# Kernel optimization log

Hardware: AMD Instinct MI355X
Metric: run time of the kernel (lower is better)

The kernel has to match this reference:

```python
import jax, jax.numpy as jnp
import numpy as np

EMBED = 1024
HEADS = 16
HEAD_DIM = EMBED // HEADS


def setup_inputs() -> dict:
    key = jax.random.key(0)
    ks = jax.random.split(key, 9)
    s = 0.02
    x = jax.random.normal(ks[0], (2, 2048, EMBED), dtype=jnp.float32)
    Wq = jax.random.normal(ks[1], (EMBED, EMBED), dtype=jnp.float32) * s
    bq = jnp.zeros((EMBED,), dtype=jnp.float32)
    Wk = jax.random.normal(ks[2], (EMBED, EMBED), dtype=jnp.float32) * s
    bk = jnp.zeros((EMBED,), dtype=jnp.float32)
    Wv = jax.random.normal(ks[3], (EMBED, EMBED), dtype=jnp.float32) * s
    bv = jnp.zeros((EMBED,), dtype=jnp.float32)
    Wo = jax.random.normal(ks[4], (EMBED, EMBED), dtype=jnp.float32) * s
    bo = jnp.zeros((EMBED,), dtype=jnp.float32)
    return {"x": x, "Wq": Wq, "bq": bq, "Wk": Wk, "bk": bk,
            "Wv": Wv, "bv": bv, "Wo": Wo, "bo": bo}


def reference(x, Wq, bq, Wk, bk, Wv, bv, Wo, bo):
    B, S, E = x.shape
    H, D = HEADS, HEAD_DIM
    scale = jnp.sqrt(jnp.asarray(D, dtype=x.dtype))
    # projections (torch Linear: y = x @ W.T + b)
    q = (x @ Wq.T + bq).reshape(B, S, H, D).transpose(0, 2, 1, 3)  # [B,H,S,D]
    k = (x @ Wk.T + bk).reshape(B, S, H, D).transpose(0, 2, 1, 3)
    v = (x @ Wv.T + bv).reshape(B, S, H, D).transpose(0, 2, 1, 3)
    scores = jnp.einsum('bhqd,bhkd->bhqk', q, k) / scale  # [B,H,S,S]
    probs = jax.nn.softmax(scores, axis=-1)
    out = jnp.einsum('bhqk,bhkd->bhqd', probs, v)  # [B,H,S,D]
    out = out.transpose(0, 2, 1, 3).reshape(B, S, E)
    return out @ Wo.T + bo
```

## Files before the change

kernel.cpp:

```cpp
#include <hip/hip_runtime.h>
#include <cstddef>

#define EMBED 1024
#define HEADS 16
#define HDIM  64
#define BATCH 2
#define SEQ   2048
#define MTOT  (BATCH*SEQ)

typedef __attribute__((ext_vector_type(8)))  short short8;
typedef __attribute__((ext_vector_type(4)))  float f32x4;
typedef __attribute__((ext_vector_type(16))) float f32x16;

typedef __attribute__((address_space(1))) const unsigned int* gas_u32p;
typedef __attribute__((address_space(3))) unsigned int* las_u32p;

static __device__ __forceinline__ void gload_lds16(const void* g, void* l) {
    __builtin_amdgcn_global_load_lds((gas_u32p)g, (las_u32p)l, 16, 0, 0);
}

static __device__ __forceinline__ unsigned short f2bf(float x) {
    unsigned u = __builtin_bit_cast(unsigned, x);
    unsigned r = (u + 0x7FFFu + ((u >> 16) & 1u)) >> 16;
    return (unsigned short)r;
}

static __device__ __forceinline__ unsigned pk_bf16(float lo, float hi) {
    unsigned r;
    asm("v_cvt_pk_bf16_f32 %0, %1, %2" : "=v"(r) : "v"(lo), "v"(hi));
    return r;
}

static __device__ __forceinline__ void plane32_swap(unsigned &a, unsigned &b) {
    auto r = __builtin_amdgcn_permlane32_swap((int)a, (int)b, false, false);
    a = (unsigned)r[0];
    b = (unsigned)r[1];
}

static __device__ __forceinline__ f32x16 mfma32(short8 a, short8 b, f32x16 c) {
    return __builtin_amdgcn_mfma_f32_32x32x16_bf16(a, b, c, 0, 0, 0);
}

__global__ __launch_bounds__(256)
void convx(const float* __restrict__ x, unsigned short* __restrict__ xh)
{
    const size_t i = ((size_t)blockIdx.x * 256 + threadIdx.x) * 8;
    float4 a = *(const float4*)(x + i);
    float4 b = *(const float4*)(x + i + 4);
    unsigned short o[8] __attribute__((aligned(16)));
    o[0] = f2bf(a.x); o[1] = f2bf(a.y); o[2] = f2bf(a.z); o[3] = f2bf(a.w);
    o[4] = f2bf(b.x); o[5] = f2bf(b.y); o[6] = f2bf(b.z); o[7] = f2bf(b.w);
    *(uint4*)(xh + i) = *(const uint4*)o;
}

__global__ __launch_bounds__(256)
void convw(const float* __restrict__ Wq, const float* __restrict__ Wk,
           const float* __restrict__ Wv, const float* __restrict__ Wo,
           unsigned short* __restrict__ Wh)
{
    const int sel = blockIdx.y;
    const float* src = sel == 0 ? Wq : sel == 1 ? Wk : sel == 2 ? Wv : Wo;
    unsigned short* dst = Wh + (size_t)sel * EMBED * EMBED;
    const size_t i = ((size_t)blockIdx.x * 256 + threadIdx.x) * 4;
    float4 a = *(const float4*)(src + i);
    ushort4 o;
    o.x = f2bf(a.x); o.y = f2bf(a.y); o.z = f2bf(a.z); o.w = f2bf(a.w);
    *(ushort4*)(dst + i) = o;
}

__global__ __launch_bounds__(256)
void gemm_qkv_bf16(const unsigned short* __restrict__ A,
                   const unsigned short* __restrict__ Wqh,
                   const unsigned short* __restrict__ Wkh,
                   const unsigned short* __restrict__ Wvh,
                   const float* __restrict__ bq,
                   const float* __restrict__ bk,
                   const float* __restrict__ bv,
                   unsigned short* __restrict__ Qb,
                   unsigned short* __restrict__ Kb,
                   unsigned short* __restrict__ Vt)
{
    __shared__ short As[128 * 32];
    __shared__ short Bs[128 * 32];

    const int tid  = threadIdx.x;
    const int lane = tid & 63;
    const int w    = tid >> 6;
    const int c    = lane & 15;
    const int g    = lane >> 4;
    const int wr   = w >> 1;
    const int wc   = w & 1;

    const int m0   = blockIdx.y * 128;
    const int bx   = blockIdx.x;
    const int wsel = bx >> 3;
    const int n0   = (bx & 7) * 128;

    const unsigned short* W = (wsel == 0) ? Wqh : (wsel == 1) ? Wkh : Wvh;
    const float* bias       = (wsel == 0) ? bq  : (wsel == 1) ? bk  : bv;

    f32x4 acc[4][4] = {};

    for (int k0 = 0; k0 < EMBED; k0 += 32) {
        __syncthreads();
        #pragma unroll
        for (int i = 0; i < 2; ++i) {
            int s   = (w * 2 + i) * 64 + lane;
            int row = s >> 2;
            int k8  = (s & 3) * 8;
            gload_lds16(A + (size_t)(m0 + row) * EMBED + k0 + k8,
                        As + (size_t)(w * 2 + i) * 512);
            gload_lds16(W + (size_t)(n0 + row) * EMBED + k0 + k8,
                        Bs + (size_t)(w * 2 + i) * 512);
        }
        __syncthreads();

        short8 af[4], bf[4];
        #pragma unroll
        for (int mi = 0; mi < 4; ++mi)
            af[mi] = *(const short8*)&As[(wr * 64 + mi * 16 + c) * 32 + g * 8];
        #pragma unroll
        for (int ni = 0; ni < 4; ++ni)
            bf[ni] = *(const short8*)&Bs[(wc * 64 + ni * 16 + c) * 32 + g * 8];
        #pragma unroll
        for (int mi = 0; mi < 4; ++mi)
            #pragma unroll
            for (int ni = 0; ni < 4; ++ni)
                acc[mi][ni] = __builtin_amdgcn_mfma_f32_16x16x32_bf16(
                    af[mi], bf[ni], acc[mi][ni], 0, 0, 0);
    }

    if (wsel == 2) {
        #pragma unroll
        for (int mi = 0; mi < 4; ++mi) {
            const int m  = m0 + wr * 64 + mi * 16 + g * 4;
            const int bb = m >> 11;
            const int ss = m & (SEQ - 1);
            #pragma unroll
            for (int ni = 0; ni < 4; ++ni) {
                const int col = n0 + wc * 64 + ni * 16 + c;
                const int hh = col >> 6, dd = col & 63;
                const float bi_ = bias[col];
                ushort4 o;
                o.x = f2bf(acc[mi][ni][0] + bi_);
                o.y = f2bf(acc[mi][ni][1] + bi_);
                o.z = f2bf(acc[mi][ni][2] + bi_);
                o.w = f2bf(acc[mi][ni][3] + bi_);
                *(ushort4*)&Vt[((size_t)((bb * HEADS + hh) * HDIM) + dd) * SEQ + ss] = o;
            }
        }
    } else {
        unsigned short* Out = (wsel == 0) ? Qb : Kb;
        const float oscale  = (wsel == 0) ? 0.125f : 1.0f;
        #pragma unroll
        for (int mi = 0; mi < 4; ++mi)
            #pragma unroll
            for (int r = 0; r < 4; ++r) {
                const int m = m0 + wr * 64 + mi * 16 + g * 4 + r;
                #pragma unroll
                for (int ni = 0; ni < 4; ++ni) {
                    const int col = n0 + wc * 64 + ni * 16 + c;
                    Out[(size_t)m * EMBED + col] =
                        f2bf((acc[mi][ni][r] + bias[col]) * oscale);
                }
            }
    }
}

__global__ __launch_bounds__(256)
void gemm_o_bf16(const unsigned short* __restrict__ A,
                 const unsigned short* __restrict__ Woh,
                 const float* __restrict__ bo,
                 float* __restrict__ C)
{
    __shared__ short As[128 * 32];
    __shared__ short Bs[64 * 32];

    const int tid  = threadIdx.x;
    const int lane = tid & 63;
    const int w    = tid >> 6;
    const int c    = lane & 15;
    const int g    = lane >> 4;
    const int wr   = w >> 1;
    const int wc   = w & 1;

    const int m0 = blockIdx.y * 128;
    const int n0 = blockIdx.x * 64;

    f32x4 acc[4][2] = {};

    for (int k0 = 0; k0 < EMBED; k0 += 32) {
        __syncthreads();
        #pragma unroll
        for (int i = 0; i < 2; ++i) {
            int s   = (w * 2 + i) * 64 + lane;
            int row = s >> 2;
            int k8  = (s & 3) * 8;
            gload_lds16(A + (size_t)(m0 + row) * EMBED + k0 + k8,
                        As + (size_t)(w * 2 + i) * 512);
        }
        {
            int s   = w * 64 + lane;
            int row = s >> 2;
            int k8  = (s & 3) * 8;
            gload_lds16(Woh + (size_t)(n0 + row) * EMBED + k0 + k8,
                        Bs + (size_t)w * 512);
        }
        __syncthreads();

        short8 af[4], bf[2];
        #pragma unroll
        for (int mi = 0; mi < 4; ++mi)
            af[mi] = *(const short8*)&As[(wr * 64 + mi * 16 + c) * 32 + g * 8];
        #pragma unroll
        for (int ni = 0; ni < 2; ++ni)
            bf[ni] = *(const short8*)&Bs[(wc * 32 + ni * 16 + c) * 32 + g * 8];
        #pragma unroll
        for (int mi = 0; mi < 4; ++mi)
            #pragma unroll
            for (int ni = 0; ni < 2; ++ni)
                acc[mi][ni] = __builtin_amdgcn_mfma_f32_16x16x32_bf16(
                    af[mi], bf[ni], acc[mi][ni], 0, 0, 0);
    }

    #pragma unroll
    for (int mi = 0; mi < 4; ++mi)
        #pragma unroll
        for (int r = 0; r < 4; ++r) {
            const int m = m0 + wr * 64 + mi * 16 + g * 4 + r;
            #pragma unroll
            for (int ni = 0; ni < 2; ++ni) {
                const int col = n0 + wc * 32 + ni * 16 + c;
                C[(size_t)m * EMBED + col] = acc[mi][ni][r] + bo[col];
            }
        }
}

__global__ __launch_bounds__(512, 4)
void flash_attn_mfma3(const unsigned short* __restrict__ Qb,
                      const unsigned short* __restrict__ Kb,
                      const unsigned short* __restrict__ Vt,
                      unsigned short* __restrict__ O)
{
    __shared__ short KT[2][2][64 * 64];
    __shared__ short VT[2][2][64 * 64];

    const int tid  = threadIdx.x;
    const int lane = tid & 63;
    const int w    = tid >> 6;
    const int qt   = w & 3;
    const int half = w >> 2;
    const int l31  = lane & 31;
    const int hi   = lane >> 5;
    const int q0   = blockIdx.x * 128 + qt * 32;
    const int h    = blockIdx.y;
    const int b    = blockIdx.z;

    short8 qf[4];
    {
        const unsigned short* qrow =
            Qb + (size_t)(b * SEQ + q0 + l31) * EMBED + h * HDIM + hi * 8;
        #pragma unroll
        for (int kc = 0; kc < 4; ++kc)
            qf[kc] = *(const short8*)(qrow + kc * 16);
    }

    const int tb     = w >> 1;
    const int sthalf = tb >> 1;
    const int stV    = tb & 1;
    const int ssub   = w & 1;
    const int strow  = ssub * 32 + (lane >> 3);
    const int ch     = (lane & 7) ^ (strow & 7);
    const unsigned short* kS =
        Kb + (size_t)(b * SEQ + sthalf * (SEQ / 2) + strow) * EMBED + h * HDIM + ch * 8;
    const unsigned short* vS =
        Vt + ((size_t)((b * HEADS + h) * HDIM) + strow) * SEQ + sthalf * (SEQ / 2) + ch * 8;

    f32x16 acc[2] = {};
    float m_run = -1e30f, l_run = 0.f;

    #define STAGE(kt2, bb)                                                    \
        do {                                                                  \
            if (stV == 0) {                                                   \
                const unsigned short* src = kS + (size_t)(kt2) * 64 * EMBED;  \
                short* kd = &KT[sthalf][bb][ssub * 2048];                     \
                _Pragma("unroll")                                             \
                for (int it = 0; it < 4; ++it)                                \
                    gload_lds16(src + (size_t)it * 8 * EMBED, kd + it * 512); \
            } else {                                                          \
                const unsigned short* src = vS + (kt2) * 64;                  \
                short* vd = &VT[sthalf][bb][ssub * 2048];                     \
                _Pragma("unroll")                                             \
                for (int it = 0; it < 4; ++it)                                \
                    gload_lds16(src + (size_t)it * 8 * SEQ, vd + it * 512);   \
            }                                                                 \
        } while (0)

    STAGE(0, 0);
    __syncthreads();

    for (int kt = 0; kt < SEQ / 2 / 64; ++kt) {
        const int bi = kt & 1;
        if (kt < SEQ / 2 / 64 - 1) STAGE(kt + 1, bi ^ 1);

        const short* kb_ = &KT[half][bi][0];
        const short* vb_ = &VT[half][bi][0];

        f32x16 s[2] = {};
        #pragma unroll
        for (int t = 0; t < 2; ++t) {
            const int row = t * 32 + l31;
            const int rm  = l31 & 7;
            #pragma unroll
            for (int kc = 0; kc < 4; ++kc) {
                short8 ka = *(const short8*)&kb_[row * 64 + (((2 * kc + hi) ^ rm) * 8)];
                s[t] = mfma32(ka, qf[kc], s[t]);
            }
        }

        float mt = -1e30f;
        #pragma unroll
        for (int t = 0; t < 2; ++t)
            #pragma unroll
            for (int r = 0; r < 16; ++r)
                mt = fmaxf(mt, s[t][r]);
        mt = fmaxf(mt, __shfl_xor(mt, 32, 64));

        if (__any(mt > m_run + 8.f)) {
            float mnew  = fmaxf(m_run, mt);
            float alpha = __expf(m_run - mnew);
            m_run = mnew;
            l_run *= alpha;
            #pragma unroll
            for (int r = 0; r < 16; ++r) {
                const int qr = (r & 3) + 8 * (r >> 2) + 4 * hi;
                float af = __shfl(alpha, qr, 64);
                acc[0][r] *= af;
                acc[1][r] *= af;
            }
        }

        float rs = 0.f;
        #pragma unroll
        for (int t = 0; t < 2; ++t)
            #pragma unroll
            for (int r = 0; r < 16; ++r) {
                float pv = __expf(s[t][r] - m_run);
                s[t][r] = pv;
                rs += pv;
            }
        rs += __shfl_xor(rs, 32, 64);
        l_run += rs;

        short8 pf[2][2];
        #pragma unroll
        for (int t = 0; t < 2; ++t)
            #pragma unroll
            for (int kc = 0; kc < 2; ++kc) {
                unsigned A0 = pk_bf16(s[t][8 * kc + 0], s[t][8 * kc + 1]);
                unsigned A1 = pk_bf16(s[t][8 * kc + 2], s[t][8 * kc + 3]);
                unsigned B0 = pk_bf16(s[t][8 * kc + 4], s[t][8 * kc + 5]);
                unsigned B1 = pk_bf16(s[t][8 * kc + 6], s[t][8 * kc + 7]);
                plane32_swap(A0, B0);
                plane32_swap(A1, B1);
                uint4 fw = make_uint4(A0, A1, B0, B1);
                pf[t][kc] = __builtin_bit_cast(short8, fw);
            }

        #pragma unroll
        for (int dt = 0; dt < 2; ++dt) {
            const int row = dt * 32 + l31;
            const int rm  = l31 & 7;
            #pragma unroll
            for (int t = 0; t < 2; ++t)
                #pragma unroll
                for (int kc = 0; kc < 2; ++kc) {
                    short8 vf = *(const short8*)
                        &vb_[row * 64 + (((4 * t + 2 * kc + hi) ^ rm) * 8)];
                    acc[dt] = mfma32(pf[t][kc], vf, acc[dt]);
                }
        }

        __syncthreads();
    }
    #undef STAGE

    float* mrgf = (float*)&KT[0][0][0];
    float* mlbf = (float*)&VT[0][0][0];
    if (half == 1) {
        #pragma unroll
        for (int dt = 0; dt < 2; ++dt)
            #pragma unroll
            for (int r = 0; r < 16; ++r) {
                const int qr = (r & 3) + 8 * (r >> 2) + 4 * hi;
                mrgf[qt * 2048 + qr * 64 + dt * 32 + l31] = acc[dt][r];
            }
        if (lane < 32) {
            *(float2*)&mlbf[qt * 64 + lane * 2] = make_float2(m_run, l_run);
        }
    }
    __syncthreads();
    if (half == 0) {
        float2 ml = *(const float2*)&mlbf[qt * 64 + l31 * 2];
        float mx  = fmaxf(m_run, ml.x);
        float al  = __expf(m_run - mx);
        float ah  = __expf(ml.x - mx);
        float inv = 1.f / (l_run * al + ml.y * ah);
        float fl = al * inv, fh = ah * inv;
        #pragma unroll
        for (int r = 0; r < 16; ++r) {
            const int qr = (r & 3) + 8 * (r >> 2) + 4 * hi;
            float flr = __shfl(fl, qr, 64);
            float fhr = __shfl(fh, qr, 64);
            #pragma unroll
            for (int dt = 0; dt < 2; ++dt) {
                float oh  = mrgf[qt * 2048 + qr * 64 + dt * 32 + l31];
                float val = acc[dt][r] * flr + oh * fhr;
                O[(size_t)(b * SEQ + q0 + qr) * EMBED + h * HDIM + dt * 32 + l31]
                    = f2bf(val);
            }
        }
    }
}

extern "C" void kernel_launch(void* const* d_in, const int* in_sizes, int n_in,
                              void* d_out, int out_size, void* d_ws, size_t ws_size,
                              hipStream_t stream)
{
    const float* x  = (const float*)d_in[0];
    const float* Wq = (const float*)d_in[1];
    const float* bq = (const float*)d_in[2];
    const float* Wk = (const float*)d_in[3];
    const float* bk = (const float*)d_in[4];
    const float* Wv = (const float*)d_in[5];
    const float* bv = (const float*)d_in[6];
    const float* Wo = (const float*)d_in[7];
    const float* bo = (const float*)d_in[8];
    float* out = (float*)d_out;

    const size_t ME = (size_t)MTOT * EMBED;
    unsigned short* xh   = (unsigned short*)d_ws;
    unsigned short* Qb   = xh   + ME;
    unsigned short* Kb   = Qb   + ME;
    unsigned short* Vt   = Kb   + ME;
    unsigned short* attn = Vt   + ME;
    unsigned short* Wh   = attn + ME;

    dim3 blk(256);

    convx<<<dim3(MTOT * EMBED / 2048), blk, 0, stream>>>(x, xh);
    convw<<<dim3(EMBED * EMBED / 1024, 4), blk, 0, stream>>>(Wq, Wk, Wv, Wo, Wh);

    gemm_qkv_bf16<<<dim3(24, MTOT / 128), blk, 0, stream>>>(
        xh, Wh, Wh + (size_t)EMBED * EMBED, Wh + 2 * (size_t)EMBED * EMBED,
        bq, bk, bv, Qb, Kb, Vt);

    flash_attn_mfma3<<<dim3(SEQ / 128, HEADS, BATCH), dim3(512), 0, stream>>>(
        Qb, Kb, Vt, attn);

    gemm_o_bf16<<<dim3(EMBED / 64, MTOT / 128), blk, 0, stream>>>(
        attn, Wh + 3 * (size_t)EMBED * EMBED, bo, out);
}
```

Measured before the change: 133.8 us.

## Split attention KV range four ways per block and widen output GEMM tile

The attention kernel moves from 512 to 1024 threads per block. Each query tile is now split across four KV quarters of 512 keys, processed in 32-key steps. The partial softmax results are combined by a two-level tree merge through LDS, and s_setprio is raised around the MFMA sections. The output projection GEMM tile grows from 128x64 to 128x128, which halves its grid and raises reuse per block. The cost is more merge synchronization and register pressure, and occupancy changes with the larger block and the launch_bounds(1024,8) hint.

```diff
diff --git a/kernel.cpp b/kernel.cpp
--- a/kernel.cpp
+++ b/kernel.cpp
@@ -174,7 +174,7 @@
                  float* __restrict__ C)
 {
     __shared__ short As[128 * 32];
-    __shared__ short Bs[64 * 32];
+    __shared__ short Bs[128 * 32];
 
     const int tid  = threadIdx.x;
     const int lane = tid & 63;
@@ -185,9 +185,9 @@
     const int wc   = w & 1;
 
     const int m0 = blockIdx.y * 128;
-    const int n0 = blockIdx.x * 64;
-
-    f32x4 acc[4][2] = {};
+    const int n0 = blockIdx.x * 128;
+
+    f32x4 acc[4][4] = {};
 
     for (int k0 = 0; k0 < EMBED; k0 += 32) {
         __syncthreads();
@@ -198,27 +198,22 @@
             int k8  = (s & 3) * 8;
             gload_lds16(A + (size_t)(m0 + row) * EMBED + k0 + k8,
                         As + (size_t)(w * 2 + i) * 512);
-        }
-        {
-            int s   = w * 64 + lane;
-            int row = s >> 2;
-            int k8  = (s & 3) * 8;
             gload_lds16(Woh + (size_t)(n0 + row) * EMBED + k0 + k8,
-                        Bs + (size_t)w * 512);
+                        Bs + (size_t)(w * 2 + i) * 512);
         }
         __syncthreads();
 
-        short8 af[4], bf[2];
+        short8 af[4], bf[4];
         #pragma unroll
         for (int mi = 0; mi < 4; ++mi)
             af[mi] = *(const short8*)&As[(wr * 64 + mi * 16 + c) * 32 + g * 8];
         #pragma unroll
-        for (int ni = 0; ni < 2; ++ni)
-            bf[ni] = *(const short8*)&Bs[(wc * 32 + ni * 16 + c) * 32 + g * 8];
+        for (int ni = 0; ni < 4; ++ni)
+            bf[ni] = *(const short8*)&Bs[(wc * 64 + ni * 16 + c) * 32 + g * 8];
         #pragma unroll
         for (int mi = 0; mi < 4; ++mi)
             #pragma unroll
-            for (int ni = 0; ni < 2; ++ni)
+            for (int ni = 0; ni < 4; ++ni)
                 acc[mi][ni] = __builtin_amdgcn_mfma_f32_16x16x32_bf16(
                     af[mi], bf[ni], acc[mi][ni], 0, 0, 0);
     }
@@ -229,29 +224,31 @@
         for (int r = 0; r < 4; ++r) {
             const int m = m0 + wr * 64 + mi * 16 + g * 4 + r;
             #pragma unroll
-            for (int ni = 0; ni < 2; ++ni) {
-                const int col = n0 + wc * 32 + ni * 16 + c;
+            for (int ni = 0; ni < 4; ++ni) {
+                const int col = n0 + wc * 64 + ni * 16 + c;
                 C[(size_t)m * EMBED + col] = acc[mi][ni][r] + bo[col];
             }
         }
 }
 
-__global__ __launch_bounds__(512, 4)
-void flash_attn_mfma3(const unsigned short* __restrict__ Qb,
+__global__ __launch_bounds__(1024, 8)
+void flash_attn_mfma4(const unsigned short* __restrict__ Qb,
                       const unsigned short* __restrict__ Kb,
                       const unsigned short* __restrict__ Vt,
                       unsigned short* __restrict__ O)
 {
-    __shared__ short KT[2][2][64 * 64];
-    __shared__ short VT[2][2][64 * 64];
+    __shared__ short KT[4][2][32 * 64];
+    __shared__ short VS[4][2][32 * 64];
+    __shared__ float MLB[2][4][32][2];
 
     const int tid  = threadIdx.x;
     const int lane = tid & 63;
     const int w    = tid >> 6;
     const int qt   = w & 3;
-    const int half = w >> 2;
+    const int qr4  = w >> 2;
     const int l31  = lane & 31;
     const int hi   = lane >> 5;
+    const int rm   = l31 & 7;
     const int q0   = blockIdx.x * 128 + qt * 32;
     const int h    = blockIdx.y;
     const int b    = blockIdx.z;
@@ -265,65 +262,61 @@
             qf[kc] = *(const short8*)(qrow + kc * 16);
     }
 
-    const int tb     = w >> 1;
-    const int sthalf = tb >> 1;
-    const int stV    = tb & 1;
-    const int ssub   = w & 1;
-    const int strow  = ssub * 32 + (lane >> 3);
-    const int ch     = (lane & 7) ^ (strow & 7);
-    const unsigned short* kS =
-        Kb + (size_t)(b * SEQ + sthalf * (SEQ / 2) + strow) * EMBED + h * HDIM + ch * 8;
-    const unsigned short* vS =
-        Vt + ((size_t)((b * HEADS + h) * HDIM) + strow) * SEQ + sthalf * (SEQ / 2) + ch * 8;
+    const int stV  = (w >> 1) & 1;
+    const int ssub = w & 1;
+    const int r0   = ssub * 16 + (lane >> 3);
+    const int r1   = r0 + 8;
+    const int sl   = lane & 7;
+    const int c0   = sl ^ (r0 & 7);
+    const int c1   = sl ^ (r1 & 7);
+    const unsigned short* g0;
+    const unsigned short* g1;
+    if (stV == 0) {
+        g0 = Kb + (size_t)(b * SEQ + qr4 * 512 + r0) * EMBED + h * HDIM + c0 * 8;
+        g1 = Kb + (size_t)(b * SEQ + qr4 * 512 + r1) * EMBED + h * HDIM + c1 * 8;
+    } else {
+        const int d0 = r0 + 32 * (c0 >> 2), k0o = (c0 & 3) * 8;
+        const int d1 = r1 + 32 * (c1 >> 2), k1o = (c1 & 3) * 8;
+        g0 = Vt + ((size_t)((b * HEADS + h) * HDIM) + d0) * SEQ + qr4 * 512 + k0o;
+        g1 = Vt + ((size_t)((b * HEADS + h) * HDIM) + d1) * SEQ + qr4 * 512 + k1o;
+    }
+    const size_t adv = (stV == 0) ? (size_t)32 * EMBED : (size_t)32;
+
+    #define STAGE(bb)                                                        \
+        do {                                                                 \
+            short* dst = (stV ? &VS[qr4][bb][0] : &KT[qr4][bb][0])           \
+                         + ssub * 1024;                                      \
+            gload_lds16(g0, dst);                                            \
+            gload_lds16(g1, dst + 512);                                      \
+            g0 += adv; g1 += adv;                                            \
+        } while (0)
 
     f32x16 acc[2] = {};
     float m_run = -1e30f, l_run = 0.f;
 
-    #define STAGE(kt2, bb)                                                    \
-        do {                                                                  \
-            if (stV == 0) {                                                   \
-                const unsigned short* src = kS + (size_t)(kt2) * 64 * EMBED;  \
-                short* kd = &KT[sthalf][bb][ssub * 2048];                     \
-                _Pragma("unroll")                                             \
-                for (int it = 0; it < 4; ++it)                                \
-                    gload_lds16(src + (size_t)it * 8 * EMBED, kd + it * 512); \
-            } else {                                                          \
-                const unsigned short* src = vS + (kt2) * 64;                  \
-                short* vd = &VT[sthalf][bb][ssub * 2048];                     \
-                _Pragma("unroll")                                             \
-                for (int it = 0; it < 4; ++it)                                \
-                    gload_lds16(src + (size_t)it * 8 * SEQ, vd + it * 512);   \
-            }                                                                 \
-        } while (0)
-
-    STAGE(0, 0);
+    STAGE(0);
     __syncthreads();
 
-    for (int kt = 0; kt < SEQ / 2 / 64; ++kt) {
+    for (int kt = 0; kt < 16; ++kt) {
         const int bi = kt & 1;
-        if (kt < SEQ / 2 / 64 - 1) STAGE(kt + 1, bi ^ 1);
-
-        const short* kb_ = &KT[half][bi][0];
-        const short* vb_ = &VT[half][bi][0];
-
-        f32x16 s[2] = {};
-        #pragma unroll
-        for (int t = 0; t < 2; ++t) {
-            const int row = t * 32 + l31;
-            const int rm  = l31 & 7;
-            #pragma unroll
-            for (int kc = 0; kc < 4; ++kc) {
-                short8 ka = *(const short8*)&kb_[row * 64 + (((2 * kc + hi) ^ rm) * 8)];
-                s[t] = mfma32(ka, qf[kc], s[t]);
-            }
-        }
+        if (kt < 15) STAGE(bi ^ 1);
+
+        const short* kb_ = &KT[qr4][bi][0];
+        const short* vb_ = &VS[qr4][bi][0];
+
+        f32x16 s = {};
+        __builtin_amdgcn_s_setprio(1);
+        #pragma unroll
+        for (int kc = 0; kc < 4; ++kc) {
+            short8 ka = *(const short8*)&kb_[l31 * 64 + (((2 * kc + hi) ^ rm) * 8)];
+            s = mfma32(ka, qf[kc], s);
+        }
+        __builtin_amdgcn_s_setprio(0);
 
         float mt = -1e30f;
         #pragma unroll
-        for (int t = 0; t < 2; ++t)
-            #pragma unroll
-            for (int r = 0; r < 16; ++r)
-                mt = fmaxf(mt, s[t][r]);
+        for (int r = 0; r < 16; ++r)
+            mt = fmaxf(mt, s[r]);
         mt = fmaxf(mt, __shfl_xor(mt, 32, 64));
 
         if (__any(mt > m_run + 8.f)) {
@@ -342,80 +335,113 @@
 
         float rs = 0.f;
         #pragma unroll
-        for (int t = 0; t < 2; ++t)
-            #pragma unroll
-            for (int r = 0; r < 16; ++r) {
-                float pv = __expf(s[t][r] - m_run);
-                s[t][r] = pv;
-                rs += pv;
-            }
+        for (int r = 0; r < 16; ++r) {
+            float pv = __expf(s[r] - m_run);
+            s[r] = pv;
+            rs += pv;
+        }
         rs += __shfl_xor(rs, 32, 64);
         l_run += rs;
 
-        short8 pf[2][2];
-        #pragma unroll
-        for (int t = 0; t < 2; ++t)
+        short8 pf[2];
+        #pragma unroll
+        for (int kc = 0; kc < 2; ++kc) {
+            unsigned A0 = pk_bf16(s[8 * kc + 0], s[8 * kc + 1]);
+            unsigned A1 = pk_bf16(s[8 * kc + 2], s[8 * kc + 3]);
+            unsigned B0 = pk_bf16(s[8 * kc + 4], s[8 * kc + 5]);
+            unsigned B1 = pk_bf16(s[8 * kc + 6], s[8 * kc + 7]);
+            plane32_swap(A0, B0);
+            plane32_swap(A1, B1);
+            uint4 fw = make_uint4(A0, A1, B0, B1);
+            pf[kc] = __builtin_bit_cast(short8, fw);
+        }
+
+        __builtin_amdgcn_s_setprio(1);
+        #pragma unroll
+        for (int dt = 0; dt < 2; ++dt)
             #pragma unroll
             for (int kc = 0; kc < 2; ++kc) {
-                unsigned A0 = pk_bf16(s[t][8 * kc + 0], s[t][8 * kc + 1]);
-                unsigned A1 = pk_bf16(s[t][8 * kc + 2], s[t][8 * kc + 3]);
-                unsigned B0 = pk_bf16(s[t][8 * kc + 4], s[t][8 * kc + 5]);
-                unsigned B1 = pk_bf16(s[t][8 * kc + 6], s[t][8 * kc + 7]);
-                plane32_swap(A0, B0);
-                plane32_swap(A1, B1);
-                uint4 fw = make_uint4(A0, A1, B0, B1);
-                pf[t][kc] = __builtin_bit_cast(short8, fw);
-            }
-
-        #pragma unroll
-        for (int dt = 0; dt < 2; ++dt) {
-            const int row = dt * 32 + l31;
-            const int rm  = l31 & 7;
-            #pragma unroll
-            for (int t = 0; t < 2; ++t)
-                #pragma unroll
-                for (int kc = 0; kc < 2; ++kc) {
-                    short8 vf = *(const short8*)
-                        &vb_[row * 64 + (((4 * t + 2 * kc + hi) ^ rm) * 8)];
-                    acc[dt] = mfma32(pf[t][kc], vf, acc[dt]);
-                }
-        }
+                short8 vf = *(const short8*)
+                    &vb_[l31 * 64 + (((dt * 4 + 2 * kc + hi) ^ rm) * 8)];
+                acc[dt] = mfma32(pf[kc], vf, acc[dt]);
+            }
+        __builtin_amdgcn_s_setprio(0);
 
         __syncthreads();
     }
     #undef STAGE
 
-    float* mrgf = (float*)&KT[0][0][0];
-    float* mlbf = (float*)&VT[0][0][0];
-    if (half == 1) {
+    float* MRG0 = (float*)&KT[0][0][0];
+    float* MRG1 = (float*)&VS[0][0][0];
+
+    if (qr4 & 1) {
+        float* M = (qr4 == 1) ? MRG0 : MRG1;
         #pragma unroll
         for (int dt = 0; dt < 2; ++dt)
             #pragma unroll
             for (int r = 0; r < 16; ++r) {
                 const int qr = (r & 3) + 8 * (r >> 2) + 4 * hi;
-                mrgf[qt * 2048 + qr * 64 + dt * 32 + l31] = acc[dt][r];
-            }
-        if (lane < 32) {
-            *(float2*)&mlbf[qt * 64 + lane * 2] = make_float2(m_run, l_run);
+                M[qt * 2048 + qr * 64 + dt * 32 + l31] = acc[dt][r];
+            }
+        if (hi == 0) {
+            MLB[qr4 >> 1][qt][l31][0] = m_run;
+            MLB[qr4 >> 1][qt][l31][1] = l_run;
         }
     }
     __syncthreads();
-    if (half == 0) {
-        float2 ml = *(const float2*)&mlbf[qt * 64 + l31 * 2];
-        float mx  = fmaxf(m_run, ml.x);
-        float al  = __expf(m_run - mx);
-        float ah  = __expf(ml.x - mx);
-        float inv = 1.f / (l_run * al + ml.y * ah);
-        float fl = al * inv, fh = ah * inv;
+    if (!(qr4 & 1)) {
+        const int sel = qr4 >> 1;
+        const float* M = (qr4 == 0) ? MRG0 : MRG1;
+        float mo = MLB[sel][qt][l31][0];
+        float lo = MLB[sel][qt][l31][1];
+        float mnew = fmaxf(m_run, mo);
+        float fa = __expf(m_run - mnew);
+        float fb = __expf(mo - mnew);
+        m_run = mnew;
+        l_run = l_run * fa + lo * fb;
         #pragma unroll
         for (int r = 0; r < 16; ++r) {
             const int qr = (r & 3) + 8 * (r >> 2) + 4 * hi;
-            float flr = __shfl(fl, qr, 64);
-            float fhr = __shfl(fh, qr, 64);
+            float far = __shfl(fa, qr, 64);
+            float fbr = __shfl(fb, qr, 64);
+            #pragma unroll
+            for (int dt = 0; dt < 2; ++dt)
+                acc[dt][r] = acc[dt][r] * far
+                           + M[qt * 2048 + qr * 64 + dt * 32 + l31] * fbr;
+        }
+    }
+    __syncthreads();
+    if (qr4 == 2) {
+        #pragma unroll
+        for (int dt = 0; dt < 2; ++dt)
+            #pragma unroll
+            for (int r = 0; r < 16; ++r) {
+                const int qr = (r & 3) + 8 * (r >> 2) + 4 * hi;
+                MRG0[qt * 2048 + qr * 64 + dt * 32 + l31] = acc[dt][r];
+            }
+        if (hi == 0) {
+            MLB[0][qt][l31][0] = m_run;
+            MLB[0][qt][l31][1] = l_run;
+        }
+    }
+    __syncthreads();
+    if (qr4 == 0) {
+        float mo = MLB[0][qt][l31][0];
+        float lo = MLB[0][qt][l31][1];
+        float mnew = fmaxf(m_run, mo);
+        float fa = __expf(m_run - mnew);
+        float fb = __expf(mo - mnew);
+        float linv = 1.f / (l_run * fa + lo * fb);
+        float fan = fa * linv, fbn = fb * linv;
+        #pragma unroll
+        for (int r = 0; r < 16; ++r) {
+            const int qr = (r & 3) + 8 * (r >> 2) + 4 * hi;
+            float far = __shfl(fan, qr, 64);
+            float fbr = __shfl(fbn, qr, 64);
             #pragma unroll
             for (int dt = 0; dt < 2; ++dt) {
-                float oh  = mrgf[qt * 2048 + qr * 64 + dt * 32 + l31];
-                float val = acc[dt][r] * flr + oh * fhr;
+                float val = acc[dt][r] * far
+                          + MRG0[qt * 2048 + qr * 64 + dt * 32 + l31] * fbr;
                 O[(size_t)(b * SEQ + q0 + qr) * EMBED + h * HDIM + dt * 32 + l31]
                     = f2bf(val);
             }
@@ -455,9 +481,9 @@
         xh, Wh, Wh + (size_t)EMBED * EMBED, Wh + 2 * (size_t)EMBED * EMBED,
         bq, bk, bv, Qb, Kb, Vt);
 
-    flash_attn_mfma3<<<dim3(SEQ / 128, HEADS, BATCH), dim3(512), 0, stream>>>(
+    flash_attn_mfma4<<<dim3(SEQ / 128, HEADS, BATCH), dim3(1024), 0, stream>>>(
         Qb, Kb, Vt, attn);
 
-    gemm_o_bf16<<<dim3(EMBED / 64, MTOT / 128), blk, 0, stream>>>(
+    gemm_o_bf16<<<dim3(EMBED / 128, MTOT / 128), blk, 0, stream>>>(
         attn, Wh + 3 * (size_t)EMBED * EMBED, bo, out);
 }
```

Result: slower. 435.5 us (+225.5%).
